# Kernel optimization log

Measured on AMD Instinct MI355X. Metric: run time of the kernel, lower is better.

Reference implementation:

```python
import jax, jax.numpy as jnp
import numpy as np


def setup_inputs() -> dict:
    key = jax.random.key(0)
    k1, k2, k3, k4 = jax.random.split(key, 4)
    B, S, E, H = 8, 2048, 4096, 128  # batch, seq, embed, head_size
    scale = 1.0 / np.sqrt(E)
    return {
        "x": jax.random.normal(k1, (B, S, E), dtype=jnp.float32),
        "Wq": jax.random.normal(k2, (E, H), dtype=jnp.float32) * scale,
        "Wk": jax.random.normal(k3, (E, H), dtype=jnp.float32) * scale,
        "Wv": jax.random.normal(k4, (E, H), dtype=jnp.float32) * scale,
    }


def reference(x, Wq, Wk, Wv):
    # Single-head attention, non-flash branch, mask=None, eval-mode dropout.
    q = jnp.einsum("bse,eh->bsh", x, Wq)  # [B,S,H]
    k = jnp.einsum("bse,eh->bsh", x, Wk)
    v = jnp.einsum("bse,eh->bsh", x, Wv)
    head_size = k.shape[-1]
    scores = jnp.einsum("bqh,bkh->bqk", q, k) * (head_size ** -0.5)  # [B,S,S]
    attn = jax.nn.softmax(scores, axis=-1)
    out = jnp.einsum("bqk,bkh->bqh", attn, v)  # [B,S,H]
    return out
```

## Files before the change

### kernel.cpp

```cpp
#include <hip/hip_runtime.h>
#include <math.h>

typedef __bf16 bf16_t;
typedef bf16_t bf16x8 __attribute__((ext_vector_type(8)));
typedef float floatx4 __attribute__((ext_vector_type(4)));

#define MFMA(a, b, c) __builtin_amdgcn_mfma_f32_16x16x32_bf16(a, b, c, 0, 0, 0)

static constexpr int S = 2048, E = 4096, H = 128;

__device__ __forceinline__ void gl_lds16(const void* g, void* l) {
  __builtin_amdgcn_global_load_lds((const __attribute__((address_space(1))) void*)g,
                                   (__attribute__((address_space(3))) void*)l,
                                   16, 0, 0);
}

__global__ __launch_bounds__(256) void wt_kernel(const float* __restrict__ Wq,
                                                 const float* __restrict__ Wk,
                                                 const float* __restrict__ Wv,
                                                 bf16_t* __restrict__ Wt) {
  __shared__ bf16_t tile[64][130];
  int wb = blockIdx.x / 64;
  int eb = blockIdx.x % 64;
  const float* W = wb == 0 ? Wq : (wb == 1 ? Wk : Wv);
  int t = threadIdx.x;
  {
    int er = t >> 2, q = t & 3;
    const float4* src = (const float4*)(W + (size_t)(eb * 64 + er) * H + q * 32);
    for (int i = 0; i < 8; ++i) {
      float4 f = src[i];
      int c = q * 32 + i * 4;
      tile[er][c + 0] = (bf16_t)f.x; tile[er][c + 1] = (bf16_t)f.y;
      tile[er][c + 2] = (bf16_t)f.z; tile[er][c + 3] = (bf16_t)f.w;
    }
  }
  __syncthreads();
  {
    int h = t >> 1, half = t & 1;
    bf16_t buf[32];
    for (int j = 0; j < 32; ++j) buf[j] = tile[half * 32 + j][h];
    bf16_t* dst = Wt + (size_t)(wb * H + h) * E + eb * 64 + half * 32;
    for (int i = 0; i < 4; ++i) ((uint4*)dst)[i] = ((uint4*)buf)[i];
  }
}

__global__ __launch_bounds__(256, 3) void qkv_kernel(const float* __restrict__ X,
                                                     const bf16_t* __restrict__ Wt,
                                                     bf16_t* __restrict__ Qb,
                                                     bf16_t* __restrict__ Kb,
                                                     bf16_t* __restrict__ Vt) {
  __shared__ __align__(16) char smem[49152];

  int phys = blockIdx.x;
  int xcd = phys & 7, slot = phys >> 3;
  int trip = slot / 3, nb = slot % 3;
  int mBase = (xcd * 32 + trip) * 64;

  int t = threadIdx.x, lane = t & 63, w = t >> 6;
  int wr = w >> 1, wc = w & 1;
  int r16 = lane & 15, q4 = lane >> 4;

  floatx4 acc[2][4] = {};

  const float* xbase = X + (size_t)mBase * E + (t & 31) * 4;
  int xrow0 = t >> 5;
  int wrow0 = lane >> 4, wg = lane & 15;

  float4 xa[8], xb[8];
#pragma unroll
  for (int i = 0; i < 8; ++i) xa[i] = *(const float4*)(xbase + (size_t)(i * 8 + xrow0) * E);

#define STAGE_W(K0)                                                              \
  _Pragma("unroll") for (int is = 0; is < 8; ++is) {                             \
    int row = w * 32 + is * 4 + wrow0;                                           \
    int g = wg ^ (row & 15);                                                     \
    gl_lds16(Wt + (size_t)(nb * 128 + row) * E + (K0) + g * 8,                   \
             smem + 16384 + (w * 32 + is * 4) * 256 + lane * 16);                \
  }

#define STAGE_X(XR)                                                              \
  _Pragma("unroll") for (int i = 0; i < 8; ++i) {                                \
    int row = i * 8 + xrow0;                                                     \
    float4 f = (XR)[i];                                                          \
    bf16_t pk[4] = {(bf16_t)f.x, (bf16_t)f.y, (bf16_t)f.z, (bf16_t)f.w};         \
    int sl = ((t & 31) >> 1) ^ (row & 15);                                       \
    *(uint2*)(smem + row * 256 + sl * 16 + (t & 1) * 8) = *(uint2*)pk;           \
  }

#define LOAD_X(XR, K0)                                                           \
  _Pragma("unroll") for (int i = 0; i < 8; ++i)                                  \
      (XR)[i] = *(const float4*)(xbase + (size_t)(i * 8 + xrow0) * E + (K0));

#define COMPUTE()                                                                \
  _Pragma("unroll") for (int kc = 0; kc < 4; ++kc) {                             \
    bf16x8 a[2], b[4];                                                           \
    _Pragma("unroll") for (int i = 0; i < 2; ++i) {                              \
      int row = wr * 32 + i * 16 + r16;                                          \
      int sl = (kc * 4 + q4) ^ r16;                                              \
      a[i] = *(const bf16x8*)(smem + row * 256 + sl * 16);                       \
    }                                                                            \
    _Pragma("unroll") for (int j = 0; j < 4; ++j) {                              \
      int row = wc * 64 + j * 16 + r16;                                          \
      int sl = (kc * 4 + q4) ^ r16;                                              \
      b[j] = *(const bf16x8*)(smem + 16384 + row * 256 + sl * 16);               \
    }                                                                            \
    _Pragma("unroll") for (int i = 0; i < 2; ++i)                                \
        _Pragma("unroll") for (int j = 0; j < 4; ++j)                            \
            acc[i][j] = MFMA(a[i], b[j], acc[i][j]);                             \
  }

  for (int kb = 0; kb < 32; kb += 2) {
    STAGE_W(kb * 128);
    STAGE_X(xa);
    __syncthreads();
    LOAD_X(xb, (kb + 1) * 128);
    COMPUTE();
    __syncthreads();

    STAGE_W((kb + 1) * 128);
    STAGE_X(xb);
    __syncthreads();
    if (kb < 30) LOAD_X(xa, (kb + 2) * 128);
    COMPUTE();
    __syncthreads();
  }

  if (nb < 2) {
    bf16_t(*Ob)[136] = (bf16_t(*)[136])smem;
#pragma unroll
    for (int i = 0; i < 2; ++i)
#pragma unroll
      for (int j = 0; j < 4; ++j)
#pragma unroll
        for (int ii = 0; ii < 4; ++ii)
          Ob[wr * 32 + i * 16 + q4 * 4 + ii][wc * 64 + j * 16 + r16] =
              (bf16_t)acc[i][j][ii];
    __syncthreads();
    bf16_t* outp = (nb == 0 ? Qb : Kb) + (size_t)mBase * H;
    int row = t >> 2, cg = t & 3;
#pragma unroll
    for (int u = 0; u < 4; ++u)
      *(uint4*)(outp + (size_t)row * H + cg * 32 + u * 8) =
          *(uint4*)&Ob[row][cg * 32 + u * 8];
  } else {
    int bb = mBase >> 11;
    int sBase = mBase & 2047;
    bf16_t* vb = Vt + (size_t)bb * H * S;
#pragma unroll
    for (int i = 0; i < 2; ++i)
#pragma unroll
      for (int j = 0; j < 4; ++j) {
        int hcol = wc * 64 + j * 16 + r16;
        int srow = sBase + wr * 32 + i * 16 + q4 * 4;
        bf16_t pk[4];
#pragma unroll
        for (int ii = 0; ii < 4; ++ii) pk[ii] = (bf16_t)acc[i][j][ii];
        *(uint2*)&vb[(size_t)hcol * S + srow] = *(uint2*)pk;
      }
  }
#undef STAGE_W
#undef STAGE_X
#undef LOAD_X
#undef COMPUTE
}

__global__ __launch_bounds__(256, 2) void attn_kernel(const bf16_t* __restrict__ Qb,
                                                      const bf16_t* __restrict__ Kb,
                                                      const bf16_t* __restrict__ Vt,
                                                      float* __restrict__ Op,
                                                      float* __restrict__ Mp,
                                                      float* __restrict__ Lp) {
  __shared__ __align__(16) char smem[41984];
  char* kbase = smem;
  char* vbase = smem + 16384;
  bf16_t(*Vl)[64] = (bf16_t(*)[64])vbase;

  int bid = blockIdx.x;
  int b = bid & 7, r = bid >> 3;
  int qt = r >> 1, half = r & 1;

  int t = threadIdx.x, lane = t & 63, wl = t >> 6;
  int r16 = lane & 15, q4 = lane >> 4;
  bf16_t(*Pl)[72] = (bf16_t(*)[72])(smem + 32768 + wl * 2304);

  bf16x8 qf[4];
  {
    const bf16_t* qp = Qb + (size_t)(b * S + qt * 64 + wl * 16 + r16) * H + q4 * 8;
#pragma unroll
    for (int c = 0; c < 4; ++c) qf[c] = *(const bf16x8*)(qp + c * 32);
  }
  floatx4 o[8] = {};
  float m_r[4], l_r[4];
#pragma unroll
  for (int ii = 0; ii < 4; ++ii) { m_r[ii] = -1e30f; l_r[ii] = 0.f; }
  const float scale = 0.08838834764831845f;

  int kr = lane >> 4, kg = lane & 15;
  int vr = lane >> 3, vg = lane & 7;

  for (int it = 0; it < 16; ++it) {
    int kt = half * 16 + it;
#pragma unroll
    for (int is = 0; is < 4; ++is) {
      int row = wl * 16 + is * 4 + kr;
      int g = kg ^ (row & 15);
      gl_lds16(Kb + (size_t)(b * S + kt * 64 + row) * H + g * 8,
               kbase + (wl * 16 + is * 4) * 256 + lane * 16);
    }
#pragma unroll
    for (int is = 0; is < 4; ++is) {
      int row = wl * 32 + is * 8 + vr;
      int g = vg ^ (row & 7);
      gl_lds16(Vt + (size_t)(b * H + row) * S + kt * 64 + g * 8,
               vbase + (wl * 32 + is * 8) * 128 + lane * 16);
    }
    __syncthreads();

    floatx4 s4[4] = {};
#pragma unroll
    for (int c = 0; c < 4; ++c)
#pragma unroll
      for (int j = 0; j < 4; ++j) {
        int row = j * 16 + r16;
        int sl = (c * 4 + q4) ^ r16;
        bf16x8 bk = *(const bf16x8*)(kbase + row * 256 + sl * 16);
        s4[j] = MFMA(qf[c], bk, s4[j]);
      }

    float p[4][4], mx[4], ls[4], alpha[4];
#pragma unroll
    for (int ii = 0; ii < 4; ++ii) mx[ii] = -1e30f;
#pragma unroll
    for (int j = 0; j < 4; ++j)
#pragma unroll
      for (int ii = 0; ii < 4; ++ii) {
        float sv = s4[j][ii] * scale;
        p[j][ii] = sv;
        mx[ii] = fmaxf(mx[ii], sv);
      }
#pragma unroll
    for (int off = 1; off <= 8; off <<= 1)
#pragma unroll
      for (int ii = 0; ii < 4; ++ii)
        mx[ii] = fmaxf(mx[ii], __shfl_xor(mx[ii], off));
#pragma unroll
    for (int ii = 0; ii < 4; ++ii) {
      float mn = fmaxf(m_r[ii], mx[ii]);
      alpha[ii] = __expf(m_r[ii] - mn);
      m_r[ii] = mn;
      ls[ii] = 0.f;
    }
#pragma unroll
    for (int j = 0; j < 4; ++j)
#pragma unroll
      for (int ii = 0; ii < 4; ++ii) {
        float e = __expf(p[j][ii] - m_r[ii]);
        ls[ii] += e;
        Pl[q4 * 4 + ii][j * 16 + r16] = (bf16_t)e;
      }
#pragma unroll
    for (int off = 1; off <= 8; off <<= 1)
#pragma unroll
      for (int ii = 0; ii < 4; ++ii) ls[ii] += __shfl_xor(ls[ii], off);
#pragma unroll
    for (int ii = 0; ii < 4; ++ii) l_r[ii] = l_r[ii] * alpha[ii] + ls[ii];
#pragma unroll
    for (int f = 0; f < 8; ++f)
#pragma unroll
      for (int ii = 0; ii < 4; ++ii) o[f][ii] *= alpha[ii];

#pragma unroll
    for (int kc = 0; kc < 2; ++kc) {
      bf16x8 pa = *(const bf16x8*)&Pl[r16][kc * 32 + q4 * 8];
#pragma unroll
      for (int f = 0; f < 8; ++f) {
        int row = f * 16 + r16;
        int sl = (kc * 4 + q4) ^ (row & 7);
        bf16x8 bv = *(const bf16x8*)&Vl[row][sl * 8];
        o[f] = MFMA(pa, bv, o[f]);
      }
    }
    __syncthreads();
  }

  int rowg = b * S + qt * 64 + wl * 16 + q4 * 4;
  float* op = Op + ((size_t)half * 16384 + rowg) * 128;
#pragma unroll
  for (int f = 0; f < 8; ++f)
#pragma unroll
    for (int ii = 0; ii < 4; ++ii)
      op[ii * 128 + f * 16 + r16] = o[f][ii];
  if (r16 == 0) {
#pragma unroll
    for (int ii = 0; ii < 4; ++ii) {
      Mp[half * 16384 + rowg + ii] = m_r[ii];
      Lp[half * 16384 + rowg + ii] = l_r[ii];
    }
  }
}

__global__ __launch_bounds__(256) void merge_kernel(const float* __restrict__ Op,
                                                    const float* __restrict__ Mp,
                                                    const float* __restrict__ Lp,
                                                    float* __restrict__ out) {
  int t = threadIdx.x;
  int row = blockIdx.x * 64 + (t >> 2);
  int c0 = (t & 3) * 32;
  float m1 = Mp[row], m2 = Mp[16384 + row];
  float l1 = Lp[row], l2 = Lp[16384 + row];
  float M = fmaxf(m1, m2);
  float e1 = __expf(m1 - M), e2 = __expf(m2 - M);
  float inv = 1.f / (e1 * l1 + e2 * l2);
  const float4* o1 = (const float4*)(Op + (size_t)row * 128 + c0);
  const float4* o2 = (const float4*)(Op + 16384ull * 128 + (size_t)row * 128 + c0);
  float4* op = (float4*)(out + (size_t)row * 128 + c0);
#pragma unroll
  for (int i = 0; i < 8; ++i) {
    float4 a = o1[i], b = o2[i];
    float4 rr;
    rr.x = (e1 * a.x + e2 * b.x) * inv;
    rr.y = (e1 * a.y + e2 * b.y) * inv;
    rr.z = (e1 * a.z + e2 * b.z) * inv;
    rr.w = (e1 * a.w + e2 * b.w) * inv;
    op[i] = rr;
  }
}

extern "C" void kernel_launch(void* const* d_in, const int* in_sizes, int n_in,
                              void* d_out, int out_size, void* d_ws, size_t ws_size,
                              hipStream_t stream) {
  const float* x = (const float*)d_in[0];
  const float* Wq = (const float*)d_in[1];
  const float* Wk = (const float*)d_in[2];
  const float* Wv = (const float*)d_in[3];
  float* out = (float*)d_out;

  bf16_t* Wt = (bf16_t*)d_ws;
  bf16_t* Qb = Wt + (size_t)384 * 4096;
  bf16_t* Kb = Qb + (size_t)16384 * 128;
  bf16_t* Vt = Kb + (size_t)16384 * 128;
  float* Op = (float*)(Vt + (size_t)8 * 128 * 2048);
  float* Mp = Op + (size_t)2 * 16384 * 128;
  float* Lp = Mp + 2 * 16384;

  wt_kernel<<<192, 256, 0, stream>>>(Wq, Wk, Wv, Wt);
  qkv_kernel<<<768, 256, 0, stream>>>(x, Wt, Qb, Kb, Vt);
  attn_kernel<<<512, 256, 0, stream>>>(Qb, Kb, Vt, Op, Mp, Lp);
  merge_kernel<<<256, 256, 0, stream>>>(Op, Mp, Lp, out);
}
```

Baseline: 458.2 us.

## Double-buffer LDS tiles in the QKV projection and attention kernels

The QKV projection kernel now uses two LDS buffers with a K-step of 64. The next X and W tiles are staged while the current tile is computed, so each step needs one barrier instead of two. The attention kernel prefetches the next K/V tile into a second LDS buffer before computing on the current one, which hides global-load latency behind the MFMA and softmax work. The cost is more LDS per block (the attention kernel grows to about 73 KB) and more loop iterations in the projection, which could limit occupancy or add loop overhead.

```diff
diff --git a/kernel.cpp b/kernel.cpp
--- a/kernel.cpp
+++ b/kernel.cpp
@@ -62,66 +62,69 @@
 
   floatx4 acc[2][4] = {};
 
-  const float* xbase = X + (size_t)mBase * E + (t & 31) * 4;
-  int xrow0 = t >> 5;
-  int wrow0 = lane >> 4, wg = lane & 15;
-
-  float4 xa[8], xb[8];
-#pragma unroll
-  for (int i = 0; i < 8; ++i) xa[i] = *(const float4*)(xbase + (size_t)(i * 8 + xrow0) * E);
-
-#define STAGE_W(K0)                                                              \
-  _Pragma("unroll") for (int is = 0; is < 8; ++is) {                             \
-    int row = w * 32 + is * 4 + wrow0;                                           \
-    int g = wg ^ (row & 15);                                                     \
+  const float* xbase = X + (size_t)(mBase + (t >> 4)) * E + (t & 15) * 4;
+  int wrow0 = lane >> 3, wg = lane & 7;
+
+  float4 xa[4], xb[4];
+
+#define LOAD_X(XR, K0)                                                           \
+  _Pragma("unroll") for (int i = 0; i < 4; ++i)                                  \
+      (XR)[i] = *(const float4*)(xbase + (size_t)(i * 16) * E + (K0));
+
+#define STAGE_W(WOFF, K0)                                                        \
+  _Pragma("unroll") for (int is = 0; is < 4; ++is) {                             \
+    int row = w * 32 + is * 8 + wrow0;                                           \
+    int g = wg ^ (row & 7);                                                      \
     gl_lds16(Wt + (size_t)(nb * 128 + row) * E + (K0) + g * 8,                   \
-             smem + 16384 + (w * 32 + is * 4) * 256 + lane * 16);                \
-  }
-
-#define STAGE_X(XR)                                                              \
-  _Pragma("unroll") for (int i = 0; i < 8; ++i) {                                \
-    int row = i * 8 + xrow0;                                                     \
+             smem + (WOFF) + (w * 32 + is * 8) * 128 + lane * 16);               \
+  }
+
+#define STAGE_X(XOFF, XR)                                                        \
+  _Pragma("unroll") for (int i = 0; i < 4; ++i) {                                \
+    int row = i * 16 + (t >> 4);                                                 \
     float4 f = (XR)[i];                                                          \
     bf16_t pk[4] = {(bf16_t)f.x, (bf16_t)f.y, (bf16_t)f.z, (bf16_t)f.w};         \
-    int sl = ((t & 31) >> 1) ^ (row & 15);                                       \
-    *(uint2*)(smem + row * 256 + sl * 16 + (t & 1) * 8) = *(uint2*)pk;           \
-  }
-
-#define LOAD_X(XR, K0)                                                           \
-  _Pragma("unroll") for (int i = 0; i < 8; ++i)                                  \
-      (XR)[i] = *(const float4*)(xbase + (size_t)(i * 8 + xrow0) * E + (K0));
-
-#define COMPUTE()                                                                \
-  _Pragma("unroll") for (int kc = 0; kc < 4; ++kc) {                             \
+    int gg = ((t & 15) >> 1) ^ (row & 7);                                        \
+    *(uint2*)(smem + (XOFF) + row * 128 + gg * 16 + (t & 1) * 8) = *(uint2*)pk;  \
+  }
+
+#define COMPUTE(XOFF, WOFF)                                                      \
+  _Pragma("unroll") for (int kc = 0; kc < 2; ++kc) {                             \
     bf16x8 a[2], b[4];                                                           \
     _Pragma("unroll") for (int i = 0; i < 2; ++i) {                              \
       int row = wr * 32 + i * 16 + r16;                                          \
-      int sl = (kc * 4 + q4) ^ r16;                                              \
-      a[i] = *(const bf16x8*)(smem + row * 256 + sl * 16);                       \
+      int sl = (kc * 4 + q4) ^ (row & 7);                                        \
+      a[i] = *(const bf16x8*)(smem + (XOFF) + row * 128 + sl * 16);              \
     }                                                                            \
     _Pragma("unroll") for (int j = 0; j < 4; ++j) {                              \
       int row = wc * 64 + j * 16 + r16;                                          \
-      int sl = (kc * 4 + q4) ^ r16;                                              \
-      b[j] = *(const bf16x8*)(smem + 16384 + row * 256 + sl * 16);               \
+      int sl = (kc * 4 + q4) ^ (row & 7);                                        \
+      b[j] = *(const bf16x8*)(smem + (WOFF) + row * 128 + sl * 16);              \
     }                                                                            \
     _Pragma("unroll") for (int i = 0; i < 2; ++i)                                \
         _Pragma("unroll") for (int j = 0; j < 4; ++j)                            \
             acc[i][j] = MFMA(a[i], b[j], acc[i][j]);                             \
   }
 
-  for (int kb = 0; kb < 32; kb += 2) {
-    STAGE_W(kb * 128);
-    STAGE_X(xa);
+  LOAD_X(xa, 0);
+  STAGE_W(8192, 0);
+  STAGE_X(0, xa);
+  LOAD_X(xb, 64);
+  __syncthreads();
+
+  for (int kb = 0; kb < 64; kb += 2) {
+    if (kb < 62) LOAD_X(xa, (kb + 2) * 64);
+    STAGE_W(32768, (kb + 1) * 64);
+    STAGE_X(24576, xb);
+    COMPUTE(0, 8192);
     __syncthreads();
-    LOAD_X(xb, (kb + 1) * 128);
-    COMPUTE();
-    __syncthreads();
-
-    STAGE_W((kb + 1) * 128);
-    STAGE_X(xb);
-    __syncthreads();
-    if (kb < 30) LOAD_X(xa, (kb + 2) * 128);
-    COMPUTE();
+
+    if (kb < 62) {
+      LOAD_X(xb, (kb + 3) * 64);
+      STAGE_W(8192, (kb + 2) * 64);
+      STAGE_X(0, xa);
+    }
+    COMPUTE(24576, 32768);
     __syncthreads();
   }
 
@@ -158,9 +161,9 @@
         *(uint2*)&vb[(size_t)hcol * S + srow] = *(uint2*)pk;
       }
   }
+#undef LOAD_X
 #undef STAGE_W
 #undef STAGE_X
-#undef LOAD_X
 #undef COMPUTE
 }
 
@@ -170,10 +173,7 @@
                                                       float* __restrict__ Op,
                                                       float* __restrict__ Mp,
                                                       float* __restrict__ Lp) {
-  __shared__ __align__(16) char smem[41984];
-  char* kbase = smem;
-  char* vbase = smem + 16384;
-  bf16_t(*Vl)[64] = (bf16_t(*)[64])vbase;
+  __shared__ __align__(16) char smem[74752];
 
   int bid = blockIdx.x;
   int b = bid & 7, r = bid >> 3;
@@ -181,7 +181,7 @@
 
   int t = threadIdx.x, lane = t & 63, wl = t >> 6;
   int r16 = lane & 15, q4 = lane >> 4;
-  bf16_t(*Pl)[72] = (bf16_t(*)[72])(smem + 32768 + wl * 2304);
+  bf16_t(*Pl)[72] = (bf16_t(*)[72])(smem + 65536 + wl * 2304);
 
   bf16x8 qf[4];
   {
@@ -198,23 +198,28 @@
   int kr = lane >> 4, kg = lane & 15;
   int vr = lane >> 3, vg = lane & 7;
 
+#define STAGE_KV(BUF, KT)                                                        \
+  _Pragma("unroll") for (int is = 0; is < 4; ++is) {                             \
+    int row = wl * 16 + is * 4 + kr;                                             \
+    int g = kg ^ (row & 15);                                                     \
+    gl_lds16(Kb + (size_t)(b * S + (KT) * 64 + row) * H + g * 8,                 \
+             smem + (BUF) + (wl * 16 + is * 4) * 256 + lane * 16);               \
+  }                                                                              \
+  _Pragma("unroll") for (int is = 0; is < 4; ++is) {                             \
+    int row = wl * 32 + is * 8 + vr;                                             \
+    int g = vg ^ (row & 7);                                                      \
+    gl_lds16(Vt + (size_t)(b * H + row) * S + (KT) * 64 + g * 8,                 \
+             smem + (BUF) + 16384 + (wl * 32 + is * 8) * 128 + lane * 16);       \
+  }
+
+  STAGE_KV(0, half * 16);
+  __syncthreads();
+
   for (int it = 0; it < 16; ++it) {
-    int kt = half * 16 + it;
-#pragma unroll
-    for (int is = 0; is < 4; ++is) {
-      int row = wl * 16 + is * 4 + kr;
-      int g = kg ^ (row & 15);
-      gl_lds16(Kb + (size_t)(b * S + kt * 64 + row) * H + g * 8,
-               kbase + (wl * 16 + is * 4) * 256 + lane * 16);
-    }
-#pragma unroll
-    for (int is = 0; is < 4; ++is) {
-      int row = wl * 32 + is * 8 + vr;
-      int g = vg ^ (row & 7);
-      gl_lds16(Vt + (size_t)(b * H + row) * S + kt * 64 + g * 8,
-               vbase + (wl * 32 + is * 8) * 128 + lane * 16);
-    }
-    __syncthreads();
+    int cur = (it & 1) << 15;
+    if (it < 15) { STAGE_KV(cur ^ 32768, half * 16 + it + 1); }
+    const char* kbase = smem + cur;
+    bf16_t(*Vl)[64] = (bf16_t(*)[64])(smem + cur + 16384);
 
     floatx4 s4[4] = {};
 #pragma unroll
@@ -282,6 +287,7 @@
     }
     __syncthreads();
   }
+#undef STAGE_KV
 
   int rowg = b * S + qt * 64 + wl * 16 + q4 * 4;
   float* op = Op + ((size_t)half * 16384 + rowg) * 128;
```

Measured after the change: 478.0 us. 1.04x slower.
